# Kernel tuning notes

Measured on AMD Instinct MI355X. Metric: run time of the kernel, lower is better.

## Reference

```python
import jax, jax.numpy as jnp
import numpy as np

N, K, D = 1000000, 8, 32


def setup_inputs() -> dict:
    key = jax.random.key(0)
    k_x, k_mu, k_phi = jax.random.split(key, 3)
    X = jax.random.normal(k_x, (N, D), dtype=jnp.float32)
    # Gaussian.__init__: mu = (rand(dims) - 0.5) * 2, sigma = eye(dims)
    mus = (jax.random.uniform(k_mu, (K, D), dtype=jnp.float32) - 0.5) * 2.0
    sigmas = jnp.broadcast_to(jnp.eye(D, dtype=jnp.float32), (K, D, D)).copy()
    # GMM.__init__: phi ~ Dirichlet(1/count); approximate with normalized uniforms
    phi_raw = jax.random.uniform(k_phi, (K,), dtype=jnp.float32) + 1e-3
    phis = phi_raw / phi_raw.sum()
    return {"X": X, "mus": mus, "sigmas": sigmas, "phis": phis}


def reference(X, mus, sigmas, phis):
    # X: [N, D], mus: [K, D], sigmas: [K, D, D], phis: [K]
    d = X.shape[1]
    inv_sigma = jnp.linalg.pinv(sigmas)                      # [K, D, D]
    _, logdet = jnp.linalg.slogdet(sigmas)                   # [K]
    log_two_pi_dims = d * jnp.log(jnp.asarray(2.0 * np.pi, dtype=X.dtype))
    log_den = 0.5 * (log_two_pi_dims + logdet)               # [K]
    diff = X[:, None, :] - mus[None, :, :]                   # [N, K, D]
    # batched Mahalanobis quadratic form: -0.5 * diff @ inv_sigma @ diff^T (diag)
    quad = -0.5 * jnp.einsum('nkd,kde,nke->nk', diff, inv_sigma, diff)  # [N, K]
    # original subtracts exp(log_den), then scales by phi per mixture
    aff = phis[None, :] * (quad - jnp.exp(log_den)[None, :])  # [N, K]
    # ExpNormalizer.exp_norm == row-wise softmax
    return jax.nn.softmax(aff, axis=1)
```

## Files before the change

### kernel.cpp

```cpp
#include <hip/hip_runtime.h>
#include <hip/hip_bf16.h>
#include <math.h>

#define DDIM 32
#define KMIX 8
#define TPW 5

typedef short bf16x8 __attribute__((ext_vector_type(8)));
typedef float f32x4 __attribute__((ext_vector_type(4)));

__device__ __forceinline__ ushort to_bf16_rne(float f) {
    unsigned u = __builtin_bit_cast(unsigned, f);
    u = (u + 0x7FFFu + ((u >> 16) & 1u)) >> 16;
    return (ushort)u;
}

__global__ __launch_bounds__(512) void gmm_prep(
    const float* __restrict__ S, const float* __restrict__ mus,
    const float* __restrict__ phis, ushort* __restrict__ Wtg,
    ushort* __restrict__ Upan, float* __restrict__ pa2, float* __restrict__ pc)
{
    __shared__ float aug[DDIM][2 * DDIM + 2];
    __shared__ float ch[DDIM][DDIM + 1];
    __shared__ float pivsave[DDIM];
    __shared__ float amuL[DDIM];
    __shared__ float logL[DDIM];
    const int k = blockIdx.x;
    const int t = threadIdx.x;
    const int r = t >> 4;
    const int c4 = t & 15;

    aug[r][c4]      = S[k * 1024 + r * 32 + c4];
    aug[r][c4 + 16] = S[k * 1024 + r * 32 + c4 + 16];
    aug[r][c4 + 32] = (c4 == r) ? 1.f : 0.f;
    aug[r][c4 + 48] = (c4 + 16 == r) ? 1.f : 0.f;
    __syncthreads();

    for (int p = 0; p < DDIM; ++p) {
        const float piv = aug[p][p];
        const float f   = aug[r][p];
        const float pr0 = aug[p][c4];
        const float pr1 = aug[p][c4 + 16];
        const float pr2 = aug[p][c4 + 32];
        const float pr3 = aug[p][c4 + 48];
        __syncthreads();
        const float ip = 1.f / piv;
        if (r == p) {
            aug[r][c4]      = pr0 * ip;
            aug[r][c4 + 16] = pr1 * ip;
            aug[r][c4 + 32] = pr2 * ip;
            aug[r][c4 + 48] = pr3 * ip;
            if (c4 == 0) pivsave[p] = piv;
        } else {
            const float fi = f * ip;
            aug[r][c4]      = fmaf(-fi, pr0, aug[r][c4]);
            aug[r][c4 + 16] = fmaf(-fi, pr1, aug[r][c4 + 16]);
            aug[r][c4 + 32] = fmaf(-fi, pr2, aug[r][c4 + 32]);
            aug[r][c4 + 48] = fmaf(-fi, pr3, aug[r][c4 + 48]);
        }
        __syncthreads();
    }

    if (t < DDIM) {
        float acc = 0.f;
        for (int d = 0; d < DDIM; ++d)
            acc = fmaf(aug[t][32 + d], mus[k * 32 + d], acc);
        amuL[t] = acc;
        logL[t] = logf(fabsf(pivsave[t]));
    }
    ch[r][c4]      = aug[r][32 + c4];
    ch[r][c4 + 16] = aug[r][48 + c4];
    __syncthreads();

    for (int j = 0; j < DDIM; ++j) {
        const float djj = ch[j][j];
        const float cr  = ch[r][j];
        const float cc0 = ch[c4][j];
        const float cc1 = ch[c4 + 16][j];
        __syncthreads();
        const float irs = rsqrtf(djj);
        const float ird = __builtin_amdgcn_rcpf(djj);
        if (c4 == j)                       ch[r][c4]      = (r >= j) ? cr * irs : 0.f;
        else if (r > j && c4 > j)          ch[r][c4]      = fmaf(-cr * ird, cc0, ch[r][c4]);
        if (c4 + 16 == j)                  ch[r][c4 + 16] = (r >= j) ? cr * irs : 0.f;
        else if (r > j && c4 + 16 > j)     ch[r][c4 + 16] = fmaf(-cr * ird, cc1, ch[r][c4 + 16]);
        __syncthreads();
    }

    {
        const int lane0 = (t >> 3) & 63, j0 = t & 7;
        const int d0 = (lane0 >> 4) * 8 + j0;
        const int e0 = lane0 & 15;
        const int e1 = 16 + e0;
        const float f0 = (d0 >= e0) ? ch[d0][e0] : 0.f;
        const float f1 = (d0 >= e1) ? ch[d0][e1] : 0.f;
        Wtg[k * 1024 + t]       = to_bf16_rne(f0);
        Wtg[k * 1024 + 512 + t] = to_bf16_rne(f1);
    }
    if (t < DDIM)
        Upan[k * 32 + t] = to_bf16_rne(phis[k] * 1.4426950408889634f * amuL[t]);
    if (k == 0 && t >= 256) Upan[t] = 0;
    if (t == 0) {
        float ldet = 0.f, muAmu = 0.f;
        for (int i = 0; i < DDIM; ++i) {
            ldet += logL[i];
            muAmu = fmaf(amuL[i], mus[k * 32 + i], muAmu);
        }
        const float eld = expf(0.5f * (DDIM * 1.8378770664093453f + ldet));
        const float LOG2E = 1.4426950408889634f;
        pa2[k] = -0.5f * phis[k] * LOG2E;
        pc[k]  = (-0.5f * phis[k] * muAmu - phis[k] * eld) * LOG2E;
    }
}

template <int CTRL>
__device__ __forceinline__ float dpp_add(float v) {
    int t = __builtin_amdgcn_update_dpp(0, __builtin_bit_cast(int, v), CTRL, 0xF, 0xF, true);
    return v + __builtin_bit_cast(float, t);
}
__device__ __forceinline__ float sel4(float a0, float a1, float a2, float a3, int r) {
    float b0 = (r & 1) ? a1 : a0;
    float b1 = (r & 1) ? a3 : a2;
    return (r & 2) ? b1 : b0;
}
__device__ __forceinline__ float bperm_f(int addr, float v) {
    return __builtin_bit_cast(float, __builtin_amdgcn_ds_bpermute(addr, __builtin_bit_cast(int, v)));
}

__global__ __launch_bounds__(256, 6) void gmm_main(
    const float* __restrict__ X, const ushort* __restrict__ Wtg,
    const ushort* __restrict__ Upan, const float* __restrict__ pa2g,
    const float* __restrict__ pcg, float* __restrict__ out, int N)
{
    __shared__ ushort wtab[KMIX * 1024];
    const int tid = threadIdx.x;
    const int lane = tid & 63;
    const int wid = tid >> 6;
    const int g = lane >> 4;
    const int c = lane & 15;
    const int rsel = c & 3;
    const int r1 = g * 4 + rsel;
    const int p = c >> 2;

    {
        const float4* src = (const float4*)Wtg;
        float4* dst = (float4*)wtab;
#pragma unroll
        for (int i = 0; i < 4; ++i) dst[tid + 256 * i] = src[tid + 256 * i];
    }

    const bf16x8 uf = *(const bf16x8*)(Upan + c * 32 + g * 8);
    float pcv0 = pcg[0], pcv1 = pcg[1], pcv2 = pcg[2], pcv3 = pcg[3];
    float pcv4 = pcg[4], pcv5 = pcg[5], pcv6 = pcg[6], pcv7 = pcg[7];
    const float m8 = fmaxf(fmaxf(fmaxf(pcv0, pcv1), fmaxf(pcv2, pcv3)),
                           fmaxf(fmaxf(pcv4, pcv5), fmaxf(pcv6, pcv7)));
    const float paA = pa2g[2 * p], paB = pa2g[2 * p + 1];
    const float pcsA = pcg[2 * p] - m8, pcsB = pcg[2 * p + 1] - m8;
    const int src_byte = (((p >> 1) * 16 + r1) << 2);

    const int ntiles = N >> 4;
    const int tile0 = (blockIdx.x * 4 + wid) * TPW;
    const float* lp = X + (size_t)tile0 * 512 + c * 32 + g * 8;
    float* op = out + (size_t)(tile0 * 16 + r1) * 8 + p * 2;

    const f32x4 zro = {0.f, 0.f, 0.f, 0.f};
    float4 a0 = {0,0,0,0}, a1 = {0,0,0,0};
    if (tile0 < ntiles) { a0 = *(const float4*)lp; a1 = *(const float4*)(lp + 4); }

    __syncthreads();

#pragma unroll
    for (int it = 0; it < TPW; ++it) {
        const int tile = tile0 + it;
        float4 b0 = a0, b1 = a1;
        if (it + 1 < TPW && tile + 1 < ntiles) {
            b0 = *(const float4*)(lp + 512);
            b1 = *(const float4*)(lp + 516);
        }
        if (tile < ntiles) {
            int4 xi;
            xi.x = __builtin_amdgcn_perm(__builtin_bit_cast(unsigned, a0.y), __builtin_bit_cast(unsigned, a0.x), 0x07060302u);
            xi.y = __builtin_amdgcn_perm(__builtin_bit_cast(unsigned, a0.w), __builtin_bit_cast(unsigned, a0.z), 0x07060302u);
            xi.z = __builtin_amdgcn_perm(__builtin_bit_cast(unsigned, a1.y), __builtin_bit_cast(unsigned, a1.x), 0x07060302u);
            xi.w = __builtin_amdgcn_perm(__builtin_bit_cast(unsigned, a1.w), __builtin_bit_cast(unsigned, a1.z), 0x07060302u);
            const bf16x8 xf = __builtin_bit_cast(bf16x8, xi);

            const f32x4 lin = __builtin_amdgcn_mfma_f32_16x16x32_bf16(uf, xf, zro, 0, 0, 0);

            int la = lane * 16;
            asm volatile("" : "+v"(la));
            const char* wb = (const char*)wtab + la;

            float qa = 0.f, qb = 0.f;
#pragma unroll
            for (int k = 0; k < KMIX; ++k) {
                const bf16x8 wf0k = *(const bf16x8*)(wb + (k * 2 + 0) * 1024);
                bf16x8 wf1k = {0, 0, 0, 0, 0, 0, 0, 0};
                if (lane >= 32)
                    wf1k = *(const bf16x8*)(wb + (k * 2 + 1) * 1024);
                f32x4 acc0 = __builtin_amdgcn_mfma_f32_16x16x32_bf16(xf, wf0k, zro, 0, 0, 0);
                f32x4 acc1 = __builtin_amdgcn_mfma_f32_16x16x32_bf16(xf, wf1k, zro, 0, 0, 0);
                float p0 = fmaf(acc1[0], acc1[0], acc0[0] * acc0[0]);
                float p1 = fmaf(acc1[1], acc1[1], acc0[1] * acc0[1]);
                float p2 = fmaf(acc1[2], acc1[2], acc0[2] * acc0[2]);
                float p3 = fmaf(acc1[3], acc1[3], acc0[3] * acc0[3]);
                p0 = dpp_add<0xB1>(p0); p0 = dpp_add<0x4E>(p0);
                p1 = dpp_add<0xB1>(p1); p1 = dpp_add<0x4E>(p1);
                p2 = dpp_add<0xB1>(p2); p2 = dpp_add<0x4E>(p2);
                p3 = dpp_add<0xB1>(p3); p3 = dpp_add<0x4E>(p3);
                float v = sel4(p0, p1, p2, p3, rsel);
                v = dpp_add<0x124>(v);
                v = dpp_add<0x128>(v);
                if ((k >> 1) == 0) { if (p == 0) { if (k & 1) qb = v; else qa = v; } }
                if ((k >> 1) == 1) { if (p == 1) { if (k & 1) qb = v; else qa = v; } }
                if ((k >> 1) == 2) { if (p == 2) { if (k & 1) qb = v; else qa = v; } }
                if ((k >> 1) == 3) { if (p == 3) { if (k & 1) qb = v; else qa = v; } }
            }

            const float l0 = bperm_f(src_byte, lin[0]);
            const float l1 = bperm_f(src_byte, lin[1]);
            const float l2 = bperm_f(src_byte, lin[2]);
            const float l3 = bperm_f(src_byte, lin[3]);
            const float lina = (p & 1) ? l2 : l0;
            const float linb = (p & 1) ? l3 : l1;
            const float aka = fmaf(paA, qa, pcsA) + lina;
            const float akb = fmaf(paB, qb, pcsB) + linb;

            const float ea = __builtin_amdgcn_exp2f(aka);
            const float eb = __builtin_amdgcn_exp2f(akb);
            float s = ea + eb;
            s = dpp_add<0x124>(s); s = dpp_add<0x128>(s);
            const float inv = __builtin_amdgcn_rcpf(s);
            *(float2*)op = make_float2(ea * inv, eb * inv);
        }
        a0 = b0; a1 = b1;
        lp += 512;
        op += 128;
    }
}

extern "C" void kernel_launch(void* const* d_in, const int* in_sizes, int n_in,
                              void* d_out, int out_size, void* d_ws, size_t ws_size,
                              hipStream_t stream) {
    const float* X    = (const float*)d_in[0];
    const float* mus  = (const float*)d_in[1];
    const float* sig  = (const float*)d_in[2];
    const float* phis = (const float*)d_in[3];
    float* out = (float*)d_out;

    float* ws    = (float*)d_ws;
    float* pa2   = ws;
    float* pc    = ws + 8;
    ushort* Upan = (ushort*)(ws + 16);
    ushort* Wtg  = (ushort*)(ws + 272);

    const int N = in_sizes[0] / DDIM;

    gmm_prep<<<KMIX, 512, 0, stream>>>(sig, mus, phis, Wtg, Upan, pa2, pc);

    const int ntiles = N >> 4;
    const int grid = (ntiles + 4 * TPW - 1) / (4 * TPW);
    gmm_main<<<grid, 256, 0, stream>>>(X, Wtg, Upan, pa2, pc, out, N);
}
```

Measured before the change: 57.24 us.

## Fold mean into Cholesky projection and drop linear-term MFMA; double tiles per wave

The quadratic form is now computed as ||L^T x - L^T mu||^2. The per-mixture offset vector L^T mu is subtracted from the MFMA outputs before squaring, which replaces the separate linear-term MFMA, the bpermute shuffles and the mu'Amu constant. Tiles per wave are doubled to amortize the shared-memory weight table load. In exchange there are more VALU adds per mixture and 16 extra registers holding offsets, which may hurt occupancy. Precision may also shift, because the offset is now in fp32 while X stays in bf16.

```diff
diff --git a/kernel.cpp b/kernel.cpp
--- a/kernel.cpp
+++ b/kernel.cpp
@@ -4,7 +4,7 @@
 
 #define DDIM 32
 #define KMIX 8
-#define TPW 5
+#define TPW 10
 
 typedef short bf16x8 __attribute__((ext_vector_type(8)));
 typedef float f32x4 __attribute__((ext_vector_type(4)));
@@ -18,13 +18,12 @@
 __global__ __launch_bounds__(512) void gmm_prep(
     const float* __restrict__ S, const float* __restrict__ mus,
     const float* __restrict__ phis, ushort* __restrict__ Wtg,
-    ushort* __restrict__ Upan, float* __restrict__ pa2, float* __restrict__ pc)
+    float* __restrict__ wvec, float* __restrict__ pa2, float* __restrict__ pc)
 {
     __shared__ float aug[DDIM][2 * DDIM + 2];
     __shared__ float ch[DDIM][DDIM + 1];
     __shared__ float pivsave[DDIM];
-    __shared__ float amuL[DDIM];
-    __shared__ float logL[DDIM];
+    __shared__ float wv[DDIM];
     const int k = blockIdx.x;
     const int t = threadIdx.x;
     const int r = t >> 4;
@@ -61,13 +60,6 @@
         __syncthreads();
     }
 
-    if (t < DDIM) {
-        float acc = 0.f;
-        for (int d = 0; d < DDIM; ++d)
-            acc = fmaf(aug[t][32 + d], mus[k * 32 + d], acc);
-        amuL[t] = acc;
-        logL[t] = logf(fabsf(pivsave[t]));
-    }
     ch[r][c4]      = aug[r][32 + c4];
     ch[r][c4 + 16] = aug[r][48 + c4];
     __syncthreads();
@@ -86,6 +78,15 @@
         else if (r > j && c4 + 16 > j)     ch[r][c4 + 16] = fmaf(-cr * ird, cc1, ch[r][c4 + 16]);
         __syncthreads();
     }
+
+    if (t < DDIM) {
+        float acc = 0.f;
+        for (int d = t; d < DDIM; ++d)
+            acc = fmaf(ch[d][t], mus[k * 32 + d], acc);
+        wv[t] = acc;
+        wvec[k * 32 + t] = acc;
+    }
+    __syncthreads();
 
     {
         const int lane0 = (t >> 3) & 63, j0 = t & 7;
@@ -97,19 +98,13 @@
         Wtg[k * 1024 + t]       = to_bf16_rne(f0);
         Wtg[k * 1024 + 512 + t] = to_bf16_rne(f1);
     }
-    if (t < DDIM)
-        Upan[k * 32 + t] = to_bf16_rne(phis[k] * 1.4426950408889634f * amuL[t]);
-    if (k == 0 && t >= 256) Upan[t] = 0;
     if (t == 0) {
-        float ldet = 0.f, muAmu = 0.f;
-        for (int i = 0; i < DDIM; ++i) {
-            ldet += logL[i];
-            muAmu = fmaf(amuL[i], mus[k * 32 + i], muAmu);
-        }
+        float ldet = 0.f;
+        for (int i = 0; i < DDIM; ++i) ldet += logf(fabsf(pivsave[i]));
         const float eld = expf(0.5f * (DDIM * 1.8378770664093453f + ldet));
         const float LOG2E = 1.4426950408889634f;
         pa2[k] = -0.5f * phis[k] * LOG2E;
-        pc[k]  = (-0.5f * phis[k] * muAmu - phis[k] * eld) * LOG2E;
+        pc[k]  = -phis[k] * eld * LOG2E;
     }
 }
 
@@ -123,13 +118,10 @@
     float b1 = (r & 1) ? a3 : a2;
     return (r & 2) ? b1 : b0;
 }
-__device__ __forceinline__ float bperm_f(int addr, float v) {
-    return __builtin_bit_cast(float, __builtin_amdgcn_ds_bpermute(addr, __builtin_bit_cast(int, v)));
-}
 
 __global__ __launch_bounds__(256, 6) void gmm_main(
     const float* __restrict__ X, const ushort* __restrict__ Wtg,
-    const ushort* __restrict__ Upan, const float* __restrict__ pa2g,
+    const float* __restrict__ wvec, const float* __restrict__ pa2g,
     const float* __restrict__ pcg, float* __restrict__ out, int N)
 {
     __shared__ ushort wtab[KMIX * 1024];
@@ -149,14 +141,18 @@
         for (int i = 0; i < 4; ++i) dst[tid + 256 * i] = src[tid + 256 * i];
     }
 
-    const bf16x8 uf = *(const bf16x8*)(Upan + c * 32 + g * 8);
+    float nw0[KMIX], nw1[KMIX];
+#pragma unroll
+    for (int k = 0; k < KMIX; ++k) {
+        nw0[k] = -wvec[k * 32 + c];
+        nw1[k] = -wvec[k * 32 + 16 + c];
+    }
     float pcv0 = pcg[0], pcv1 = pcg[1], pcv2 = pcg[2], pcv3 = pcg[3];
     float pcv4 = pcg[4], pcv5 = pcg[5], pcv6 = pcg[6], pcv7 = pcg[7];
     const float m8 = fmaxf(fmaxf(fmaxf(pcv0, pcv1), fmaxf(pcv2, pcv3)),
                            fmaxf(fmaxf(pcv4, pcv5), fmaxf(pcv6, pcv7)));
     const float paA = pa2g[2 * p], paB = pa2g[2 * p + 1];
     const float pcsA = pcg[2 * p] - m8, pcsB = pcg[2 * p + 1] - m8;
-    const int src_byte = (((p >> 1) * 16 + r1) << 2);
 
     const int ntiles = N >> 4;
     const int tile0 = (blockIdx.x * 4 + wid) * TPW;
@@ -185,8 +181,6 @@
             xi.w = __builtin_amdgcn_perm(__builtin_bit_cast(unsigned, a1.w), __builtin_bit_cast(unsigned, a1.z), 0x07060302u);
             const bf16x8 xf = __builtin_bit_cast(bf16x8, xi);
 
-            const f32x4 lin = __builtin_amdgcn_mfma_f32_16x16x32_bf16(uf, xf, zro, 0, 0, 0);
-
             int la = lane * 16;
             asm volatile("" : "+v"(la));
             const char* wb = (const char*)wtab + la;
@@ -200,10 +194,14 @@
                     wf1k = *(const bf16x8*)(wb + (k * 2 + 1) * 1024);
                 f32x4 acc0 = __builtin_amdgcn_mfma_f32_16x16x32_bf16(xf, wf0k, zro, 0, 0, 0);
                 f32x4 acc1 = __builtin_amdgcn_mfma_f32_16x16x32_bf16(xf, wf1k, zro, 0, 0, 0);
-                float p0 = fmaf(acc1[0], acc1[0], acc0[0] * acc0[0]);
-                float p1 = fmaf(acc1[1], acc1[1], acc0[1] * acc0[1]);
-                float p2 = fmaf(acc1[2], acc1[2], acc0[2] * acc0[2]);
-                float p3 = fmaf(acc1[3], acc1[3], acc0[3] * acc0[3]);
+                const float d00 = acc0[0] + nw0[k], d10 = acc1[0] + nw1[k];
+                const float d01 = acc0[1] + nw0[k], d11 = acc1[1] + nw1[k];
+                const float d02 = acc0[2] + nw0[k], d12 = acc1[2] + nw1[k];
+                const float d03 = acc0[3] + nw0[k], d13 = acc1[3] + nw1[k];
+                float p0 = fmaf(d10, d10, d00 * d00);
+                float p1 = fmaf(d11, d11, d01 * d01);
+                float p2 = fmaf(d12, d12, d02 * d02);
+                float p3 = fmaf(d13, d13, d03 * d03);
                 p0 = dpp_add<0xB1>(p0); p0 = dpp_add<0x4E>(p0);
                 p1 = dpp_add<0xB1>(p1); p1 = dpp_add<0x4E>(p1);
                 p2 = dpp_add<0xB1>(p2); p2 = dpp_add<0x4E>(p2);
@@ -217,15 +215,8 @@
                 if ((k >> 1) == 3) { if (p == 3) { if (k & 1) qb = v; else qa = v; } }
             }
 
-            const float l0 = bperm_f(src_byte, lin[0]);
-            const float l1 = bperm_f(src_byte, lin[1]);
-            const float l2 = bperm_f(src_byte, lin[2]);
-            const float l3 = bperm_f(src_byte, lin[3]);
-            const float lina = (p & 1) ? l2 : l0;
-            const float linb = (p & 1) ? l3 : l1;
-            const float aka = fmaf(paA, qa, pcsA) + lina;
-            const float akb = fmaf(paB, qb, pcsB) + linb;
-
+            const float aka = fmaf(paA, qa, pcsA);
+            const float akb = fmaf(paB, qb, pcsB);
             const float ea = __builtin_amdgcn_exp2f(aka);
             const float eb = __builtin_amdgcn_exp2f(akb);
             float s = ea + eb;
@@ -251,14 +242,14 @@
     float* ws    = (float*)d_ws;
     float* pa2   = ws;
     float* pc    = ws + 8;
-    ushort* Upan = (ushort*)(ws + 16);
+    float* wvec  = ws + 16;
     ushort* Wtg  = (ushort*)(ws + 272);
 
     const int N = in_sizes[0] / DDIM;
-
-    gmm_prep<<<KMIX, 512, 0, stream>>>(sig, mus, phis, Wtg, Upan, pa2, pc);
-
     const int ntiles = N >> 4;
+
+    gmm_prep<<<KMIX, 512, 0, stream>>>(sig, mus, phis, Wtg, wvec, pa2, pc);
+
     const int grid = (ntiles + 4 * TPW - 1) / (4 * TPW);
-    gmm_main<<<grid, 256, 0, stream>>>(X, Wtg, Upan, pa2, pc, out, N);
-}
+    gmm_main<<<grid, 256, 0, stream>>>(X, Wtg, wvec, pa2, pc, out, N);
+}
```

Result: slower. 68.56 us (+19.8%).

## Replace Gauss-Jordan inverse plus Cholesky with LDL-based factor and double tiles per wave

Applied to the files above, without the earlier changes.

The prep kernel now does only forward elimination (an LDL^T-style factorisation) instead of full Gauss-Jordan inversion followed by a separate Cholesky of the inverse. The weight factor, the mu projection and the log-determinant now come straight from the scaled lower-triangular inverse, which removes one whole 32-step synchronised loop. Because the factor is now upper rather than lower triangular, the main kernel's masked half-load moves from the second MFMA operand to the first. Tiles per wave go from 5 to 10, which halves the grid and gives each block more work to amortise setup, at the risk of worse load balance across CUs.

```diff
diff --git a/kernel.cpp b/kernel.cpp
--- a/kernel.cpp
+++ b/kernel.cpp
@@ -4,7 +4,7 @@
 
 #define DDIM 32
 #define KMIX 8
-#define TPW 5
+#define TPW 10
 
 typedef short bf16x8 __attribute__((ext_vector_type(8)));
 typedef float f32x4 __attribute__((ext_vector_type(4)));
@@ -21,10 +21,9 @@
     ushort* __restrict__ Upan, float* __restrict__ pa2, float* __restrict__ pc)
 {
     __shared__ float aug[DDIM][2 * DDIM + 2];
-    __shared__ float ch[DDIM][DDIM + 1];
     __shared__ float pivsave[DDIM];
-    __shared__ float amuL[DDIM];
-    __shared__ float logL[DDIM];
+    __shared__ float irts[DDIM];
+    __shared__ float wv[DDIM];
     const int k = blockIdx.x;
     const int t = threadIdx.x;
     const int r = t >> 4;
@@ -44,72 +43,60 @@
         const float pr2 = aug[p][c4 + 32];
         const float pr3 = aug[p][c4 + 48];
         __syncthreads();
-        const float ip = 1.f / piv;
-        if (r == p) {
-            aug[r][c4]      = pr0 * ip;
-            aug[r][c4 + 16] = pr1 * ip;
-            aug[r][c4 + 32] = pr2 * ip;
-            aug[r][c4 + 48] = pr3 * ip;
-            if (c4 == 0) pivsave[p] = piv;
-        } else {
-            const float fi = f * ip;
+        if (r > p) {
+            const float fi = f * __builtin_amdgcn_rcpf(piv);
             aug[r][c4]      = fmaf(-fi, pr0, aug[r][c4]);
             aug[r][c4 + 16] = fmaf(-fi, pr1, aug[r][c4 + 16]);
             aug[r][c4 + 32] = fmaf(-fi, pr2, aug[r][c4 + 32]);
             aug[r][c4 + 48] = fmaf(-fi, pr3, aug[r][c4 + 48]);
         }
+        if (t == (p << 4)) pivsave[p] = piv;
         __syncthreads();
     }
+
+    if (t < DDIM) irts[t] = rsqrtf(pivsave[t]);
+    __syncthreads();
 
     if (t < DDIM) {
         float acc = 0.f;
-        for (int d = 0; d < DDIM; ++d)
+        for (int d = 0; d <= t; ++d)
             acc = fmaf(aug[t][32 + d], mus[k * 32 + d], acc);
-        amuL[t] = acc;
-        logL[t] = logf(fabsf(pivsave[t]));
-    }
-    ch[r][c4]      = aug[r][32 + c4];
-    ch[r][c4 + 16] = aug[r][48 + c4];
-    __syncthreads();
-
-    for (int j = 0; j < DDIM; ++j) {
-        const float djj = ch[j][j];
-        const float cr  = ch[r][j];
-        const float cc0 = ch[c4][j];
-        const float cc1 = ch[c4 + 16][j];
-        __syncthreads();
-        const float irs = rsqrtf(djj);
-        const float ird = __builtin_amdgcn_rcpf(djj);
-        if (c4 == j)                       ch[r][c4]      = (r >= j) ? cr * irs : 0.f;
-        else if (r > j && c4 > j)          ch[r][c4]      = fmaf(-cr * ird, cc0, ch[r][c4]);
-        if (c4 + 16 == j)                  ch[r][c4 + 16] = (r >= j) ? cr * irs : 0.f;
-        else if (r > j && c4 + 16 > j)     ch[r][c4 + 16] = fmaf(-cr * ird, cc1, ch[r][c4 + 16]);
-        __syncthreads();
-    }
+        wv[t] = acc * irts[t];
+    }
+    __syncthreads();
+
+    if (t < DDIM) {
+        float acc = 0.f;
+        for (int e = t; e < DDIM; ++e)
+            acc = fmaf(aug[e][32 + t] * irts[e], wv[e], acc);
+        Upan[k * 32 + t] = to_bf16_rne(phis[k] * 1.4426950408889634f * acc);
+    }
+    if (k == 0 && t >= 256) Upan[t] = 0;
 
     {
         const int lane0 = (t >> 3) & 63, j0 = t & 7;
         const int d0 = (lane0 >> 4) * 8 + j0;
         const int e0 = lane0 & 15;
         const int e1 = 16 + e0;
-        const float f0 = (d0 >= e0) ? ch[d0][e0] : 0.f;
-        const float f1 = (d0 >= e1) ? ch[d0][e1] : 0.f;
+        const float f0 = (d0 <= e0) ? aug[e0][32 + d0] * irts[e0] : 0.f;
+        const float f1 = (d0 <= e1) ? aug[e1][32 + d0] * irts[e1] : 0.f;
         Wtg[k * 1024 + t]       = to_bf16_rne(f0);
         Wtg[k * 1024 + 512 + t] = to_bf16_rne(f1);
     }
-    if (t < DDIM)
-        Upan[k * 32 + t] = to_bf16_rne(phis[k] * 1.4426950408889634f * amuL[t]);
-    if (k == 0 && t >= 256) Upan[t] = 0;
-    if (t == 0) {
-        float ldet = 0.f, muAmu = 0.f;
-        for (int i = 0; i < DDIM; ++i) {
-            ldet += logL[i];
-            muAmu = fmaf(amuL[i], mus[k * 32 + i], muAmu);
-        }
-        const float eld = expf(0.5f * (DDIM * 1.8378770664093453f + ldet));
-        const float LOG2E = 1.4426950408889634f;
-        pa2[k] = -0.5f * phis[k] * LOG2E;
-        pc[k]  = (-0.5f * phis[k] * muAmu - phis[k] * eld) * LOG2E;
+
+    if (t < 64) {
+        float l  = (t < DDIM) ? logf(pivsave[t]) : 0.f;
+        float w2 = (t < DDIM) ? wv[t] * wv[t] : 0.f;
+        for (int off = 32; off; off >>= 1) {
+            l  += __shfl_xor(l, off, 64);
+            w2 += __shfl_xor(w2, off, 64);
+        }
+        if (t == 0) {
+            const float eld = expf(0.5f * (DDIM * 1.8378770664093453f + l));
+            const float LOG2E = 1.4426950408889634f;
+            pa2[k] = -0.5f * phis[k] * LOG2E;
+            pc[k]  = (-0.5f * phis[k] * w2 - phis[k] * eld) * LOG2E;
+        }
     }
 }
 
@@ -194,10 +181,10 @@
             float qa = 0.f, qb = 0.f;
 #pragma unroll
             for (int k = 0; k < KMIX; ++k) {
-                const bf16x8 wf0k = *(const bf16x8*)(wb + (k * 2 + 0) * 1024);
-                bf16x8 wf1k = {0, 0, 0, 0, 0, 0, 0, 0};
-                if (lane >= 32)
-                    wf1k = *(const bf16x8*)(wb + (k * 2 + 1) * 1024);
+                bf16x8 wf0k = {0, 0, 0, 0, 0, 0, 0, 0};
+                if (lane < 32)
+                    wf0k = *(const bf16x8*)(wb + (k * 2 + 0) * 1024);
+                const bf16x8 wf1k = *(const bf16x8*)(wb + (k * 2 + 1) * 1024);
                 f32x4 acc0 = __builtin_amdgcn_mfma_f32_16x16x32_bf16(xf, wf0k, zro, 0, 0, 0);
                 f32x4 acc1 = __builtin_amdgcn_mfma_f32_16x16x32_bf16(xf, wf1k, zro, 0, 0, 0);
                 float p0 = fmaf(acc1[0], acc1[0], acc0[0] * acc0[0]);
@@ -255,10 +242,10 @@
     ushort* Wtg  = (ushort*)(ws + 272);
 
     const int N = in_sizes[0] / DDIM;
+    const int ntiles = N >> 4;
 
     gmm_prep<<<KMIX, 512, 0, stream>>>(sig, mus, phis, Wtg, Upan, pa2, pc);
 
-    const int ntiles = N >> 4;
     const int grid = (ntiles + 4 * TPW - 1) / (4 * TPW);
     gmm_main<<<grid, 256, 0, stream>>>(X, Wtg, Upan, pa2, pc, out, N);
 }
```

Result: faster. 53.50 us (median of 2 runs) (-6.5%).
